# Performance work log

Measured on AMD Instinct MI355X. Metric: run time of the kernel, lower is better.

Reference implementation:

```python
import jax, jax.numpy as jnp
import numpy as np

THRESH = 0.3
VRESET = 0.0
TAU_M = 3.0
MAX_D = 5
LENS = 0.5  # surrogate-gradient window half-width

B, WIN, N_IN = 512, 100, 700
H1, H2, H3 = 512, 256, 128

@jax.custom_vjp
def spike_fn(mem):
    # Heaviside spike with rectangular surrogate gradient (standard ActFun in SNN repos)
    return (mem > THRESH).astype(mem.dtype)

def _spike_fwd(mem):
    return spike_fn(mem), mem

def _spike_bwd(mem, g):
    return (g * (jnp.abs(mem - THRESH) < LENS).astype(g.dtype),)

spike_fn.defvjp(_spike_fwd, _spike_bwd)


def mem_update(i_spike, o_spike, mem, W, alpha):
    # mem = mem*alpha*(1-o_spike) + W @ i_spike - o_spike*vreset
    mem = mem * alpha * (1.0 - o_spike) + i_spike @ W.T - o_spike * VRESET
    s = spike_fn(mem)
    mem = mem * (mem < THRESH).astype(mem.dtype)  # hard reset above threshold
    return mem, s


def setup_inputs() -> dict:
    key = jax.random.key(0)
    ks = jax.random.split(key, 7)
    x = (jax.random.uniform(ks[0], (B, WIN, N_IN), jnp.float32) > 0.9).astype(jnp.float32)

    def lin(k, fan_out, fan_in):
        bound = 1.0 / np.sqrt(fan_in)
        return jax.random.uniform(k, (fan_out, fan_in), jnp.float32, -bound, bound)

    return {
        "x": x,
        "W_ih1": lin(ks[1], H1, N_IN),
        "W_h1h2": lin(ks[2], H2, H1),
        "W_h2h3": lin(ks[3], H3, H2),
        "W_h3h2": lin(ks[4], H2, H3),
        "W_h2h1": lin(ks[5], H1, H2),
        "W_h1o": lin(ks[6], N_IN, H1),
    }


def reference(x, W_ih1, W_h1h2, W_h2h3, W_h3h2, W_h2h1, W_h1o):
    b, t, n = x.shape
    alpha = jnp.exp(jnp.asarray(-1.0 / TAU_M, x.dtype))
    ext = jnp.concatenate([jnp.zeros((b, MAX_D, n), x.dtype), x], axis=1)  # [B, T+max_d, N]
    xs = jnp.swapaxes(ext, 0, 1)  # [T+max_d, B, N]

    z = lambda d: jnp.zeros((b, d), x.dtype)
    carry0 = (z(H1), z(H1), z(H2), z(H2), z(H3), z(H3),
              z(H2), z(H2), z(H1), z(H1), z(n), z(n))

    def step(carry, xt):
        m1, s1, m2, s2, m3, s3, m2d, s2d, m1d, s1d, mo, so = carry
        m1, s1 = mem_update(xt, s1, m1, W_ih1, alpha)
        m2, s2 = mem_update(s1, s2, m2, W_h1h2, alpha)
        m3, s3 = mem_update(s2, s3, m3, W_h2h3, alpha)
        m2d, s2d = mem_update(s3, s2d, m2d, W_h3h2, alpha)
        m1d, s1d = mem_update(s2d, s1d, m1d, W_h2h1, alpha)
        mo, so = mem_update(s1d, so, mo, W_h1o, alpha)
        return (m1, s1, m2, s2, m3, s3, m2d, s2d, m1d, s1d, mo, so), so

    _, all_o = jax.lax.scan(step, carry0, xs)  # [T+max_d, B, N]
    return jnp.swapaxes(all_o[MAX_D:], 0, 1)   # [B, T, N]
```

## Files before the change

kernel.cpp:

```cpp
#include <hip/hip_runtime.h>
#include <cmath>

namespace {

constexpr int kWin = 100;
constexpr int kNin = 700;
constexpr int kMaxD = 5;
constexpr int kT = kWin + kMaxD;

constexpr size_t OFF1 = 0;
constexpr size_t OFF2 = 358400;
constexpr size_t OFF3 = 489472;
constexpr size_t OFF4 = 522240;
constexpr size_t OFF5 = 555008;
constexpr size_t OFF6 = 686080;

__global__ void transpose_k(const float* __restrict__ src, float* __restrict__ dst,
                            int H, int K) {
  int idx = blockIdx.x * blockDim.x + threadIdx.x;
  if (idx < H * K) {
    int h = idx / K;
    int k = idx - h * K;
    dst[k * H + h] = src[idx];
  }
}

template <int NS>
__device__ __forceinline__ int compact_list(const bool* pred, int* dstList,
                                            int (*woff)[3][4], int half, int ht,
                                            int lane, int wv) {
  unsigned long long mask[NS];
#pragma unroll
  for (int c = 0; c < NS; ++c) {
    mask[c] = __ballot(pred[c]);
    if (lane == 0) woff[half][c][wv] = (int)__popcll(mask[c]);
  }
  __syncthreads();
  const unsigned long long lt = (1ull << lane) - 1ull;
  int base = 0;
#pragma unroll
  for (int c = 0; c < NS; ++c) {
    const int w0 = woff[half][c][0];
    const int w1 = woff[half][c][1];
    const int w2 = woff[half][c][2];
    const int w3 = woff[half][c][3];
    int off = base;
    if (wv > 0) off += w0;
    if (wv > 1) off += w1;
    if (wv > 2) off += w2;
    off += (int)__popcll(mask[c] & lt);
    if (pred[c]) dstList[off] = c * 256 + ht;
    base += w0 + w1 + w2 + w3;
  }
  __syncthreads();
  return base;
}

template <int K, int H, bool BUILD>
__device__ __forceinline__ int layer_step(const float* __restrict__ WT,
                                          const int* __restrict__ listIn, int cntIn,
                                          double* mem, double alpha,
                                          int* listOut, int (*woff)[3][4],
                                          int half, int ht, int lane, int wv,
                                          float* outRow, bool writeOut) {
  constexpr int NS = (H + 255) / 256;
  double acc[NS];
#pragma unroll
  for (int s = 0; s < NS; ++s) acc[s] = 0.0;

  int j = 0;
  const int cnt4 = cntIn & ~3;
  for (; j < cnt4; j += 4) {
    const int k0 = listIn[j + 0];
    const int k1 = listIn[j + 1];
    const int k2 = listIn[j + 2];
    const int k3 = listIn[j + 3];
    const float* p0 = WT + (size_t)k0 * H;
    const float* p1 = WT + (size_t)k1 * H;
    const float* p2 = WT + (size_t)k2 * H;
    const float* p3 = WT + (size_t)k3 * H;
#pragma unroll
    for (int s = 0; s < NS; ++s) {
      const int h = s * 256 + ht;
      if (h < H) {
        const float f0 = p0[h];
        const float f1 = p1[h];
        const float f2 = p2[h];
        const float f3 = p3[h];
        acc[s] += (double)f0;
        acc[s] += (double)f1;
        acc[s] += (double)f2;
        acc[s] += (double)f3;
      }
    }
  }
  for (; j < cntIn; ++j) {
    const int k0 = listIn[j];
    const float* p0 = WT + (size_t)k0 * H;
#pragma unroll
    for (int s = 0; s < NS; ++s) {
      const int h = s * 256 + ht;
      if (h < H) acc[s] += (double)p0[h];
    }
  }

  bool pred[NS];
#pragma unroll
  for (int s = 0; s < NS; ++s) {
    const int h = s * 256 + ht;
    if (h < H) {
      const double m = mem[s] * alpha + acc[s];
      const bool sp = (m > 0.3);
      pred[s] = sp;
      mem[s] = (m < 0.3) ? m : 0.0;
      if (!BUILD) {
        if (writeOut) outRow[h] = sp ? 1.0f : 0.0f;
      }
    } else {
      pred[s] = false;
    }
  }
  if (BUILD) {
    return compact_list<NS>(pred, listOut, woff, half, ht, lane, wv);
  }
  return 0;
}

__global__ __launch_bounds__(512) void snn_main(const float* __restrict__ x,
                                                const float* __restrict__ ws,
                                                float* __restrict__ out) {
  const int tid = threadIdx.x;
  const int half = tid >> 8;
  const int ht = tid & 255;
  const int lane = tid & 63;
  const int wv = (tid >> 6) & 3;
  const int row = blockIdx.x * 2 + half;

  const float* WT1 = ws + OFF1;
  const float* WT2 = ws + OFF2;
  const float* WT3 = ws + OFF3;
  const float* WT4 = ws + OFF4;
  const float* WT5 = ws + OFF5;
  const float* WT6 = ws + OFF6;

  __shared__ int lists[2][2][704];
  __shared__ int woff[2][3][4];

  double m1[2] = {0.0, 0.0};
  double m2[1] = {0.0};
  double m3[1] = {0.0};
  double m4[1] = {0.0};
  double m5[2] = {0.0, 0.0};
  double m6[3] = {0.0, 0.0, 0.0};

  const double alpha = exp(-1.0 / 3.0);

  const float* xRow = x + (size_t)row * kWin * kNin;
  float* outRowBase = out + (size_t)row * kWin * kNin;

  for (int t = 0; t < kT; ++t) {
    const bool live = (t >= kMaxD);
    int cntIn;
    {
      bool pred[3];
      if (live) {
        const float* xr = xRow + (size_t)(t - kMaxD) * kNin;
#pragma unroll
        for (int s = 0; s < 3; ++s) {
          const int h = s * 256 + ht;
          pred[s] = (h < kNin) ? (xr[h] != 0.0f) : false;
        }
      } else {
        pred[0] = pred[1] = pred[2] = false;
      }
      cntIn = compact_list<3>(pred, lists[0][half], woff, half, ht, lane, wv);
    }

    const int c1 = layer_step<700, 512, true>(WT1, lists[0][half], cntIn, m1, alpha,
                                              lists[1][half], woff, half, ht, lane, wv,
                                              nullptr, false);
    const int c2 = layer_step<512, 256, true>(WT2, lists[1][half], c1, m2, alpha,
                                              lists[0][half], woff, half, ht, lane, wv,
                                              nullptr, false);
    const int c3 = layer_step<256, 128, true>(WT3, lists[0][half], c2, m3, alpha,
                                              lists[1][half], woff, half, ht, lane, wv,
                                              nullptr, false);
    const int c4 = layer_step<128, 256, true>(WT4, lists[1][half], c3, m4, alpha,
                                              lists[0][half], woff, half, ht, lane, wv,
                                              nullptr, false);
    const int c5 = layer_step<256, 512, true>(WT5, lists[0][half], c4, m5, alpha,
                                              lists[1][half], woff, half, ht, lane, wv,
                                              nullptr, false);
    float* outRow = outRowBase + (size_t)(live ? (t - kMaxD) : 0) * kNin;
    layer_step<512, 700, false>(WT6, lists[1][half], c5, m6, alpha,
                                nullptr, woff, half, ht, lane, wv,
                                outRow, live);
  }
}

}

extern "C" void kernel_launch(void* const* d_in, const int* in_sizes, int n_in,
                              void* d_out, int out_size, void* d_ws, size_t ws_size,
                              hipStream_t stream) {
  const float* x = (const float*)d_in[0];
  float* ws = (float*)d_ws;
  float* out = (float*)d_out;

  struct TK { int H, K; size_t off; int idx; };
  const TK tk[6] = {
      {512, 700, OFF1, 1},
      {256, 512, OFF2, 2},
      {128, 256, OFF3, 3},
      {256, 128, OFF4, 4},
      {512, 256, OFF5, 5},
      {700, 512, OFF6, 6},
  };
  for (int i = 0; i < 6; ++i) {
    const int n = tk[i].H * tk[i].K;
    transpose_k<<<(n + 255) / 256, 256, 0, stream>>>(
        (const float*)d_in[tk[i].idx], ws + tk[i].off, tk[i].H, tk[i].K);
  }

  snn_main<<<256, 512, 0, stream>>>(x, ws, out);
}
```

Baseline: 1.228 ms.

## Split K across four warp-groups per row using bitmask spike sets

Replaces the shared-memory compacted spike lists with 32-bit spike bitmasks. Each batch row now gets a 1024-thread block in which four groups split the input dimension in strided 32-wide chunks, and partial sums are reduced through shared memory. Input spikes are packed into bitmasks by a separate pre-pass kernel, and the leading zero-input steps are skipped because they cannot change state. This removes the serial prefix-sum compaction and raises parallelism per row, at the cost of an extra kernel, more shared memory for double-precision partials, and a reduction barrier per layer.

```diff
diff --git a/kernel.cpp b/kernel.cpp
--- a/kernel.cpp
+++ b/kernel.cpp
@@ -5,8 +5,6 @@
 
 constexpr int kWin = 100;
 constexpr int kNin = 700;
-constexpr int kMaxD = 5;
-constexpr int kT = kWin + kMaxD;
 
 constexpr size_t OFF1 = 0;
 constexpr size_t OFF2 = 358400;
@@ -14,6 +12,8 @@
 constexpr size_t OFF4 = 522240;
 constexpr size_t OFF5 = 555008;
 constexpr size_t OFF6 = 686080;
+constexpr size_t OFF_END = 1044480;
+constexpr size_t XM_OFF_U64 = OFF_END / 2;
 
 __global__ void transpose_k(const float* __restrict__ src, float* __restrict__ dst,
                             int H, int K) {
@@ -25,126 +25,128 @@
   }
 }
 
-template <int NS>
-__device__ __forceinline__ int compact_list(const bool* pred, int* dstList,
-                                            int (*woff)[3][4], int half, int ht,
-                                            int lane, int wv) {
-  unsigned long long mask[NS];
-#pragma unroll
-  for (int c = 0; c < NS; ++c) {
-    mask[c] = __ballot(pred[c]);
-    if (lane == 0) woff[half][c][wv] = (int)__popcll(mask[c]);
-  }
+__global__ __launch_bounds__(256) void xmask_k(const float* __restrict__ x,
+                                               unsigned long long* __restrict__ xm) {
+  const int bid = blockIdx.x;
+  const int tid = threadIdx.x;
+  const int lane = tid & 63;
+  const int wv = tid >> 6;
+  const float* xr = x + (size_t)bid * kNin;
+  unsigned long long* dst = xm + (size_t)bid * 12;
+#pragma unroll
+  for (int s = 0; s < 3; ++s) {
+    const int h = s * 256 + tid;
+    const bool p = (h < kNin) ? (xr[h] != 0.0f) : false;
+    const unsigned long long b = __ballot(p);
+    if (lane == 0) dst[s * 4 + wv] = b;
+  }
+}
+
+template <int K, int H, bool BUILD, typename FCh>
+__device__ __forceinline__ void lif(const float* __restrict__ WT, FCh&& chunk,
+                                    double* mem, unsigned long long* mOut,
+                                    double (*part)[3][256],
+                                    float* outRow,
+                                    int kp, int ht, int lane, int wv4,
+                                    double alpha) {
+  constexpr int NS = (H + 255) / 256;
+  constexpr int NC = (K + 31) / 32;
+  double acc[NS];
+#pragma unroll
+  for (int s = 0; s < NS; ++s) acc[s] = 0.0;
+
+  for (int c = kp; c < NC; c += 4) {
+    unsigned m = __builtin_amdgcn_readfirstlane(chunk(c));
+    const float* __restrict__ cbase = WT + (size_t)c * 32 * H;
+    const int cnt = __builtin_popcount(m);
+    int i = 0;
+    for (; i + 4 <= cnt; i += 4) {
+      const int b0 = __builtin_ctz(m); m &= m - 1;
+      const int b1 = __builtin_ctz(m); m &= m - 1;
+      const int b2 = __builtin_ctz(m); m &= m - 1;
+      const int b3 = __builtin_ctz(m); m &= m - 1;
+      const float* p0 = cbase + b0 * H;
+      const float* p1 = cbase + b1 * H;
+      const float* p2 = cbase + b2 * H;
+      const float* p3 = cbase + b3 * H;
+#pragma unroll
+      for (int s = 0; s < NS; ++s) {
+        constexpr bool kFull = true;
+        (void)kFull;
+        const int h = s * 256 + ht;
+        if ((s + 1) * 256 <= H || h < H) {
+          const float f0 = p0[h];
+          const float f1 = p1[h];
+          const float f2 = p2[h];
+          const float f3 = p3[h];
+          acc[s] += (double)f0;
+          acc[s] += (double)f1;
+          acc[s] += (double)f2;
+          acc[s] += (double)f3;
+        }
+      }
+    }
+    for (; i < cnt; ++i) {
+      const int b0 = __builtin_ctz(m); m &= m - 1;
+      const float* p0 = cbase + b0 * H;
+#pragma unroll
+      for (int s = 0; s < NS; ++s) {
+        const int h = s * 256 + ht;
+        if ((s + 1) * 256 <= H || h < H) acc[s] += (double)p0[h];
+      }
+    }
+  }
+
+#pragma unroll
+  for (int s = 0; s < NS; ++s) part[kp][s][ht] = acc[s];
   __syncthreads();
-  const unsigned long long lt = (1ull << lane) - 1ull;
-  int base = 0;
-#pragma unroll
-  for (int c = 0; c < NS; ++c) {
-    const int w0 = woff[half][c][0];
-    const int w1 = woff[half][c][1];
-    const int w2 = woff[half][c][2];
-    const int w3 = woff[half][c][3];
-    int off = base;
-    if (wv > 0) off += w0;
-    if (wv > 1) off += w1;
-    if (wv > 2) off += w2;
-    off += (int)__popcll(mask[c] & lt);
-    if (pred[c]) dstList[off] = c * 256 + ht;
-    base += w0 + w1 + w2 + w3;
-  }
-  __syncthreads();
-  return base;
-}
-
-template <int K, int H, bool BUILD>
-__device__ __forceinline__ int layer_step(const float* __restrict__ WT,
-                                          const int* __restrict__ listIn, int cntIn,
-                                          double* mem, double alpha,
-                                          int* listOut, int (*woff)[3][4],
-                                          int half, int ht, int lane, int wv,
-                                          float* outRow, bool writeOut) {
-  constexpr int NS = (H + 255) / 256;
-  double acc[NS];
-#pragma unroll
-  for (int s = 0; s < NS; ++s) acc[s] = 0.0;
-
-  int j = 0;
-  const int cnt4 = cntIn & ~3;
-  for (; j < cnt4; j += 4) {
-    const int k0 = listIn[j + 0];
-    const int k1 = listIn[j + 1];
-    const int k2 = listIn[j + 2];
-    const int k3 = listIn[j + 3];
-    const float* p0 = WT + (size_t)k0 * H;
-    const float* p1 = WT + (size_t)k1 * H;
-    const float* p2 = WT + (size_t)k2 * H;
-    const float* p3 = WT + (size_t)k3 * H;
-#pragma unroll
-    for (int s = 0; s < NS; ++s) {
-      const int h = s * 256 + ht;
-      if (h < H) {
-        const float f0 = p0[h];
-        const float f1 = p1[h];
-        const float f2 = p2[h];
-        const float f3 = p3[h];
-        acc[s] += (double)f0;
-        acc[s] += (double)f1;
-        acc[s] += (double)f2;
-        acc[s] += (double)f3;
-      }
-    }
-  }
-  for (; j < cntIn; ++j) {
-    const int k0 = listIn[j];
-    const float* p0 = WT + (size_t)k0 * H;
-#pragma unroll
-    for (int s = 0; s < NS; ++s) {
-      const int h = s * 256 + ht;
-      if (h < H) acc[s] += (double)p0[h];
-    }
-  }
 
   bool pred[NS];
 #pragma unroll
   for (int s = 0; s < NS; ++s) {
     const int h = s * 256 + ht;
-    if (h < H) {
-      const double m = mem[s] * alpha + acc[s];
-      const bool sp = (m > 0.3);
-      pred[s] = sp;
-      mem[s] = (m < 0.3) ? m : 0.0;
+    if ((s + 1) * 256 <= H || h < H) {
+      const double p01 = part[0][s][ht] + part[1][s][ht];
+      const double tot = (p01 + part[2][s][ht]) + part[3][s][ht];
+      const double mm = mem[s] * alpha + tot;
+      pred[s] = (mm > 0.3);
+      mem[s] = (mm < 0.3) ? mm : 0.0;
       if (!BUILD) {
-        if (writeOut) outRow[h] = sp ? 1.0f : 0.0f;
+        if (kp == s) outRow[h] = pred[s] ? 1.0f : 0.0f;
       }
     } else {
       pred[s] = false;
     }
   }
   if (BUILD) {
-    return compact_list<NS>(pred, listOut, woff, half, ht, lane, wv);
-  }
-  return 0;
-}
-
-__global__ __launch_bounds__(512) void snn_main(const float* __restrict__ x,
-                                                const float* __restrict__ ws,
-                                                float* __restrict__ out) {
+#pragma unroll
+    for (int s = 0; s < NS; ++s) {
+      const unsigned long long b = __ballot(pred[s]);
+      if (kp == 0 && lane == 0) mOut[s * 4 + wv4] = b;
+    }
+    __syncthreads();
+  }
+}
+
+__global__ __launch_bounds__(1024, 8) void snn_main(
+    const float* __restrict__ wsf, const unsigned long long* __restrict__ xmask,
+    float* __restrict__ out) {
   const int tid = threadIdx.x;
-  const int half = tid >> 8;
+  const int kp = tid >> 8;
   const int ht = tid & 255;
   const int lane = tid & 63;
-  const int wv = (tid >> 6) & 3;
-  const int row = blockIdx.x * 2 + half;
-
-  const float* WT1 = ws + OFF1;
-  const float* WT2 = ws + OFF2;
-  const float* WT3 = ws + OFF3;
-  const float* WT4 = ws + OFF4;
-  const float* WT5 = ws + OFF5;
-  const float* WT6 = ws + OFF6;
-
-  __shared__ int lists[2][2][704];
-  __shared__ int woff[2][3][4];
+  const int wv4 = (tid >> 6) & 3;
+  const int row = blockIdx.x;
+
+  const float* WT1 = wsf + OFF1;
+  const float* WT2 = wsf + OFF2;
+  const float* WT3 = wsf + OFF3;
+  const float* WT4 = wsf + OFF4;
+  const float* WT5 = wsf + OFF5;
+  const float* WT6 = wsf + OFF6;
+
+  __shared__ unsigned long long mk[2][12];
+  __shared__ double parts[2][4][3][256];
 
   double m1[2] = {0.0, 0.0};
   double m2[1] = {0.0};
@@ -155,46 +157,27 @@
 
   const double alpha = exp(-1.0 / 3.0);
 
-  const float* xRow = x + (size_t)row * kWin * kNin;
+  const unsigned long long* xmRow = xmask + (size_t)row * kWin * 12;
   float* outRowBase = out + (size_t)row * kWin * kNin;
 
-  for (int t = 0; t < kT; ++t) {
-    const bool live = (t >= kMaxD);
-    int cntIn;
-    {
-      bool pred[3];
-      if (live) {
-        const float* xr = xRow + (size_t)(t - kMaxD) * kNin;
-#pragma unroll
-        for (int s = 0; s < 3; ++s) {
-          const int h = s * 256 + ht;
-          pred[s] = (h < kNin) ? (xr[h] != 0.0f) : false;
-        }
-      } else {
-        pred[0] = pred[1] = pred[2] = false;
-      }
-      cntIn = compact_list<3>(pred, lists[0][half], woff, half, ht, lane, wv);
-    }
-
-    const int c1 = layer_step<700, 512, true>(WT1, lists[0][half], cntIn, m1, alpha,
-                                              lists[1][half], woff, half, ht, lane, wv,
-                                              nullptr, false);
-    const int c2 = layer_step<512, 256, true>(WT2, lists[1][half], c1, m2, alpha,
-                                              lists[0][half], woff, half, ht, lane, wv,
-                                              nullptr, false);
-    const int c3 = layer_step<256, 128, true>(WT3, lists[0][half], c2, m3, alpha,
-                                              lists[1][half], woff, half, ht, lane, wv,
-                                              nullptr, false);
-    const int c4 = layer_step<128, 256, true>(WT4, lists[1][half], c3, m4, alpha,
-                                              lists[0][half], woff, half, ht, lane, wv,
-                                              nullptr, false);
-    const int c5 = layer_step<256, 512, true>(WT5, lists[0][half], c4, m5, alpha,
-                                              lists[1][half], woff, half, ht, lane, wv,
-                                              nullptr, false);
-    float* outRow = outRowBase + (size_t)(live ? (t - kMaxD) : 0) * kNin;
-    layer_step<512, 700, false>(WT6, lists[1][half], c5, m6, alpha,
-                                nullptr, woff, half, ht, lane, wv,
-                                outRow, live);
+  for (int t = 0; t < kWin; ++t) {
+    const unsigned* xm32 = (const unsigned*)(xmRow + (size_t)t * 12);
+    const unsigned* mk0 = (const unsigned*)&mk[0][0];
+    const unsigned* mk1 = (const unsigned*)&mk[1][0];
+
+    lif<700, 512, true>(WT1, [&](int c) { return xm32[c]; }, m1, mk[0],
+                        parts[0], nullptr, kp, ht, lane, wv4, alpha);
+    lif<512, 256, true>(WT2, [&](int c) { return mk0[c]; }, m2, mk[1],
+                        parts[1], nullptr, kp, ht, lane, wv4, alpha);
+    lif<256, 128, true>(WT3, [&](int c) { return mk1[c]; }, m3, mk[0],
+                        parts[0], nullptr, kp, ht, lane, wv4, alpha);
+    lif<128, 256, true>(WT4, [&](int c) { return mk0[c]; }, m4, mk[1],
+                        parts[1], nullptr, kp, ht, lane, wv4, alpha);
+    lif<256, 512, true>(WT5, [&](int c) { return mk1[c]; }, m5, mk[0],
+                        parts[0], nullptr, kp, ht, lane, wv4, alpha);
+    float* outRow = outRowBase + (size_t)t * kNin;
+    lif<512, 700, false>(WT6, [&](int c) { return mk0[c]; }, m6, nullptr,
+                         parts[1], outRow, kp, ht, lane, wv4, alpha);
   }
 }
 
@@ -205,6 +188,7 @@
                               hipStream_t stream) {
   const float* x = (const float*)d_in[0];
   float* ws = (float*)d_ws;
+  unsigned long long* xm = (unsigned long long*)d_ws + XM_OFF_U64;
   float* out = (float*)d_out;
 
   struct TK { int H, K; size_t off; int idx; };
@@ -222,5 +206,7 @@
         (const float*)d_in[tk[i].idx], ws + tk[i].off, tk[i].H, tk[i].K);
   }
 
-  snn_main<<<256, 512, 0, stream>>>(x, ws, out);
-}
+  xmask_k<<<512 * kWin, 256, 0, stream>>>(x, xm);
+
+  snn_main<<<512, 1024, 0, stream>>>(ws, xm, out);
+}
```

Measured after the change: 1.125 ms. -8.4%, faster.
